# Kernel tuning notes

Hardware: AMD Instinct MI355X
Metric: run time of the kernel (lower is better)

## Reference

```python
import jax, jax.numpy as jnp
import numpy as np


def setup_inputs() -> dict:
    key = jax.random.key(0)
    k_x, k_w, k_b = jax.random.split(key, 3)
    B, Cin, H, W = 32, 256, 56, 56
    Cout, KH, KW = 256, 3, 3
    x = jax.random.normal(k_x, (B, Cin, H, W), dtype=jnp.float32)
    fp_weight = jax.random.normal(k_w, (Cout, Cin, KH, KW), dtype=jnp.float32)
    # binary quantization, conv_mode='input_ch': per-output-channel scale
    scaling_factors = jnp.mean(jnp.abs(fp_weight), axis=(1, 2, 3), keepdims=True)  # [Cout,1,1,1]
    quant_weights = jnp.sign(fp_weight)  # values in {-1,0,1}
    bias = jax.random.normal(k_b, (Cout,), dtype=jnp.float32)
    return {"x": x, "scaling_factors": scaling_factors,
            "quant_weights": quant_weights, "bias": bias}


def reference(x, scaling_factors, quant_weights, bias):
    # Dequantize: per-out-channel scale times sign weights
    new_weights = scaling_factors * quant_weights  # [Cout,Cin,3,3]
    out = jax.lax.conv_general_dilated(
        x, new_weights,
        window_strides=(1, 1),
        padding=((1, 1), (1, 1)),
        dimension_numbers=("NCHW", "OIHW", "NCHW"),
    )
    return out + bias[None, :, None, None]
```

## Files before the change

### kernel.cpp

```cpp
#include <hip/hip_runtime.h>

using half8   = __attribute__((ext_vector_type(8))) _Float16;
using floatx4 = __attribute__((ext_vector_type(4))) float;
using floatx2 = __attribute__((ext_vector_type(2))) float;
using short8  = __attribute__((ext_vector_type(8))) short;

#define XT_ROW_ELEMS 2560
#define XT_ROW_BYTES 5120
#define XT_OFF ((size_t)2 << 20)
#define XT_BYTES ((size_t)256 * 58 * XT_ROW_BYTES)

__device__ __forceinline__ void dma16(const void* g, void* l) {
  __builtin_amdgcn_global_load_lds(
      (const __attribute__((address_space(1))) void*)g,
      (__attribute__((address_space(3))) void*)l, 16, 0, 0);
}

__global__ __launch_bounds__(256) void prep_kernel(
    const float* __restrict__ x, const float* __restrict__ qw,
    _Float16* __restrict__ wre, _Float16* __restrict__ xt)
{
  const int bid = blockIdx.x;
  const int t = threadIdx.x;
  if (bid >= 14848) {
    int idx = (bid - 14848) * 256 + t;
    int c = idx & 255, co = (idx >> 8) & 255, s = idx >> 16;
    wre[idx] = (_Float16)qw[(co * 256 + c) * 9 + s];
    return;
  }
  __shared__ _Float16 lt[32 * 57];
  const int hh = bid % 58;
  const int bc = bid / 58;
  const int cc = bc & 7, b = bc >> 3;
  _Float16* dst = xt + ((size_t)bc * 58 + hh) * XT_ROW_ELEMS;
  const bool interior = (hh >= 1) && (hh <= 56);
  if (interior) {
    const int c = t >> 3, j = t & 7;
    const float* src = x + (((size_t)(b * 256 + cc * 32 + c)) * 56 + (hh - 1)) * 56 + j * 7;
#pragma unroll
    for (int i = 0; i < 7; ++i) lt[c * 57 + j * 7 + i] = (_Float16)src[i];
  }
  __syncthreads();
  for (int ch = t; ch < 320; ch += 256) {
    int pos = ch / 5, sl = ch - pos * 5;
    short8 v = {0, 0, 0, 0, 0, 0, 0, 0};
    if (interior && sl < 4 && pos >= 1 && pos <= 56) {
      int w = pos - 1;
#pragma unroll
      for (int i = 0; i < 8; ++i)
        v[i] = __builtin_bit_cast(short, lt[(sl * 8 + i) * 57 + w]);
    }
    *reinterpret_cast<short8*>(dst + ch * 8) = v;
  }
}

__global__ __launch_bounds__(256, 4) void binconv_v3(
    const float* __restrict__ scale, const float* __restrict__ bias,
    const _Float16* __restrict__ wre, const _Float16* __restrict__ xt,
    float* __restrict__ out)
{
  __shared__ _Float16 xs[2 * 4 * 64 * 40];

  const int tid    = threadIdx.x;
  const int bid    = blockIdx.x;
  const int cohalf = bid & 1;
  const int nb     = bid >> 1;
  const int b      = nb / 28;
  const int h0     = (nb % 28) * 2;
  const int wave   = tid >> 6;
  const int lane   = tid & 63;
  const int nl     = lane & 15;
  const int quad   = lane >> 4;
  const int co_wave = cohalf * 128 + wave * 32;

  int bbase[7];
#pragma unroll
  for (int j = 0; j < 7; ++j) {
    int n = j * 16 + nl;
    int r = (n >= 56) ? 1 : 0;
    int w = n - r * 56;
    bbase[j] = (r * 64 + w) * 80 + quad * 16;
  }

  const _Float16* aptr[2];
#pragma unroll
  for (int mi = 0; mi < 2; ++mi)
    aptr[mi] = wre + (co_wave + mi * 16 + nl) * 256 + quad * 8;

  floatx4 acc[2][7];
#pragma unroll
  for (int mi = 0; mi < 2; ++mi)
#pragma unroll
    for (int j = 0; j < 7; ++j)
      acc[mi][j] = (floatx4){0.f, 0.f, 0.f, 0.f};

  const char* xsrc = (const char*)(xt + ((size_t)(b * 8) * 58 + h0) * XT_ROW_ELEMS);
  const int wlane = wave * XT_ROW_BYTES + lane * 16;
  const int wldso = wave * XT_ROW_BYTES;

#pragma unroll
  for (int i = 0; i < 5; ++i)
    dma16(xsrc + wlane + i * 1024, (char*)xs + wldso + i * 1024);

  int bufoff = 0;
  for (int cc = 0; cc < 8; ++cc) {
    __syncthreads();
    if (cc < 7) {
      const char* srcn = xsrc + (size_t)(cc + 1) * (58 * XT_ROW_BYTES);
#pragma unroll
      for (int i = 0; i < 5; ++i)
        dma16(srcn + wlane + i * 1024,
              (char*)xs + (bufoff ^ 20480) + wldso + i * 1024);
    }
    const int c0 = cc * 32;
    const char* xb = (const char*)xs + bufoff;
    __builtin_amdgcn_s_setprio(1);
#pragma unroll
    for (int s = 0; s < 9; ++s) {
      const int kh = s / 3, kw = s - kh * 3;
      half8 a[2];
#pragma unroll
      for (int mi = 0; mi < 2; ++mi)
        a[mi] = *reinterpret_cast<const half8*>(aptr[mi] + s * 65536 + c0);
      const int soff = (kh * 64 + kw) * 80;
#pragma unroll
      for (int j = 0; j < 7; ++j) {
        half8 bf = *reinterpret_cast<const half8*>(xb + bbase[j] + soff);
#pragma unroll
        for (int mi = 0; mi < 2; ++mi)
          acc[mi][j] = __builtin_amdgcn_mfma_f32_16x16x32_f16(a[mi], bf, acc[mi][j], 0, 0, 0);
      }
    }
    __builtin_amdgcn_s_setprio(0);
    bufoff ^= 20480;
  }

#pragma unroll
  for (int mi = 0; mi < 2; ++mi) {
#pragma unroll
    for (int reg = 0; reg < 4; ++reg) {
      int co = co_wave + mi * 16 + quad * 4 + reg;
      float s_ = scale[co];
      float bi = bias[co];
#pragma unroll
      for (int j = 0; j < 7; ++j) {
        int n = j * 16 + nl;
        int r = (n >= 56) ? 1 : 0;
        int w = n - r * 56;
        out[(((size_t)b * 256 + co) * 56 + (h0 + r)) * 56 + w] =
            acc[mi][j][reg] * s_ + bi;
      }
    }
  }
}

__global__ void repack_weights(const float* __restrict__ qw,
                               _Float16* __restrict__ wre, int n) {
  int t = blockIdx.x * 256 + threadIdx.x;
  if (t >= n) return;
  int c = t & 255, co = (t >> 8) & 255, s = t >> 16;
  wre[t] = (_Float16)qw[(co * 256 + c) * 9 + s];
}

__global__ __launch_bounds__(512, 4) void binconv_fused(
    const float* __restrict__ x, const float* __restrict__ scale,
    const float* __restrict__ bias, const _Float16* __restrict__ wre,
    float* __restrict__ out)
{
  __shared__ _Float16 xs[2 * 4 * 64 * 40];
  const int tid  = threadIdx.x;
  const int nb   = blockIdx.x;
  const int b    = nb / 28;
  const int h0   = (nb % 28) * 2;
  const int wave = tid >> 6;
  const int lane = tid & 63;
  const int nl   = lane & 15;
  const int quad = lane >> 4;
  const int co_wave = wave * 32;
  {
    short8 z = {0, 0, 0, 0, 0, 0, 0, 0};
    short8* xs8 = reinterpret_cast<short8*>(xs);
#pragma unroll
    for (int i = 0; i < 5; ++i) xs8[tid + i * 512] = z;
  }
  const int r     = wave >> 1;
  const int chalf = wave & 1;
  const int sc    = lane & 15;
  const int q     = lane >> 4;
  const int ch    = chalf * 16 + sc;
  const int w0    = q * 14;
  const int h     = h0 + r - 1;
  const bool hok  = (h >= 0) && (h < 56);
  const float* xc = x + (((size_t)b * 256 + ch) * 56 + (hok ? h : 0)) * 56 + w0;
  _Float16* const wrow = xs + r * 2560 + ch;
  floatx2 va[7];
  int bbase[7];
#pragma unroll
  for (int j = 0; j < 7; ++j) {
    int n = j * 16 + nl;
    int rr = (n >= 56) ? 1 : 0;
    int w = n - rr * 56;
    bbase[j] = (rr * 64 + w) * 80 + quad * 16;
  }
  const _Float16* aptr[2];
#pragma unroll
  for (int mi = 0; mi < 2; ++mi)
    aptr[mi] = wre + (co_wave + mi * 16 + nl) * 256 + quad * 8;
  floatx4 acc[2][7];
#pragma unroll
  for (int mi = 0; mi < 2; ++mi)
#pragma unroll
    for (int j = 0; j < 7; ++j)
      acc[mi][j] = (floatx4){0.f, 0.f, 0.f, 0.f};
  __syncthreads();
  if (hok) {
#pragma unroll
    for (int i = 0; i < 7; ++i)
      va[i] = *reinterpret_cast<const floatx2*>(xc + 2 * i);
#pragma unroll
    for (int i = 0; i < 7; ++i) {
      wrow[(w0 + 2 * i + 1) * 40] = (_Float16)va[i][0];
      wrow[(w0 + 2 * i + 2) * 40] = (_Float16)va[i][1];
    }
  }
  int bufe = 0;
  for (int cc = 0; cc < 8; ++cc) {
    __syncthreads();
    if (cc < 7 && hok) {
      const float* A = xc + (size_t)(cc + 1) * 100352;
#pragma unroll
      for (int i = 0; i < 7; ++i)
        va[i] = *reinterpret_cast<const floatx2*>(A + 2 * i);
    }
    const int c0 = cc * 32;
    const char* xb = reinterpret_cast<const char*>(xs) + bufe * 2;
#pragma unroll
    for (int s = 0; s < 9; ++s) {
      const int kh = s / 3, kw = s - kh * 3;
      half8 a[2];
#pragma unroll
      for (int mi = 0; mi < 2; ++mi)
        a[mi] = *reinterpret_cast<const half8*>(aptr[mi] + s * 65536 + c0);
      const int soff = (kh * 64 + kw) * 80;
#pragma unroll
      for (int j = 0; j < 7; ++j) {
        half8 bf = *reinterpret_cast<const half8*>(xb + bbase[j] + soff);
#pragma unroll
        for (int mi = 0; mi < 2; ++mi)
          acc[mi][j] = __builtin_amdgcn_mfma_f32_16x16x32_f16(a[mi], bf, acc[mi][j], 0, 0, 0);
      }
    }
    if (cc < 7 && hok) {
      _Float16* d = wrow + (bufe ^ 10240);
#pragma unroll
      for (int i = 0; i < 7; ++i) {
        d[(w0 + 2 * i + 1) * 40] = (_Float16)va[i][0];
        d[(w0 + 2 * i + 2) * 40] = (_Float16)va[i][1];
      }
    }
    bufe ^= 10240;
  }
#pragma unroll
  for (int mi = 0; mi < 2; ++mi) {
#pragma unroll
    for (int reg = 0; reg < 4; ++reg) {
      int co = co_wave + mi * 16 + quad * 4 + reg;
      float s_ = scale[co];
      float bi = bias[co];
#pragma unroll
      for (int j = 0; j < 7; ++j) {
        int n = j * 16 + nl;
        int rr = (n >= 56) ? 1 : 0;
        int w = n - rr * 56;
        out[(((size_t)b * 256 + co) * 56 + (h0 + rr)) * 56 + w] =
            acc[mi][j][reg] * s_ + bi;
      }
    }
  }
}

extern "C" void kernel_launch(void* const* d_in, const int* in_sizes, int n_in,
                              void* d_out, int out_size, void* d_ws, size_t ws_size,
                              hipStream_t stream) {
  const float* x     = (const float*)d_in[0];
  const float* scale = (const float*)d_in[1];
  const float* qw    = (const float*)d_in[2];
  const float* bias  = (const float*)d_in[3];
  float* out = (float*)d_out;

  _Float16* wre = (_Float16*)d_ws;

  if (ws_size >= XT_OFF + XT_BYTES) {
    _Float16* xt = (_Float16*)((char*)d_ws + XT_OFF);
    prep_kernel<<<17152, 256, 0, stream>>>(x, qw, wre, xt);
    binconv_v3<<<1792, 256, 0, stream>>>(scale, bias, wre, xt, out);
  } else {
    repack_weights<<<2304, 256, 0, stream>>>(qw, wre, 9 * 256 * 256);
    binconv_fused<<<896, 512, 0, stream>>>(x, scale, bias, wre, out);
  }
}
```

Baseline: 341.2 us.

## Double per-wave output-channel tile and software-pipeline operand loads in binconv

Each block now covers all 256 output channels (64 per wave) instead of splitting them across two blocks, so every LDS input tile is staged once and reused across twice as many MFMAs. The grid is halved and launch bounds drop to 2 blocks per SM to make room for the larger accumulator set. The weight and LDS operand loads are also prefetched one kernel tap ahead into register double-buffers, overlapping them with the MFMAs of the current tap. The cost is higher register pressure and lower occupancy, and the 896-block grid may fill the 256 CUs unevenly.

```diff
diff --git a/kernel.cpp b/kernel.cpp
--- a/kernel.cpp
+++ b/kernel.cpp
@@ -54,24 +54,22 @@
   }
 }
 
-__global__ __launch_bounds__(256, 4) void binconv_v3(
+__global__ __launch_bounds__(256, 2) void binconv_v4(
     const float* __restrict__ scale, const float* __restrict__ bias,
     const _Float16* __restrict__ wre, const _Float16* __restrict__ xt,
     float* __restrict__ out)
 {
   __shared__ _Float16 xs[2 * 4 * 64 * 40];
 
-  const int tid    = threadIdx.x;
-  const int bid    = blockIdx.x;
-  const int cohalf = bid & 1;
-  const int nb     = bid >> 1;
-  const int b      = nb / 28;
-  const int h0     = (nb % 28) * 2;
-  const int wave   = tid >> 6;
-  const int lane   = tid & 63;
-  const int nl     = lane & 15;
-  const int quad   = lane >> 4;
-  const int co_wave = cohalf * 128 + wave * 32;
+  const int tid  = threadIdx.x;
+  const int nb   = blockIdx.x;
+  const int b    = nb / 28;
+  const int h0   = (nb % 28) * 2;
+  const int wave = tid >> 6;
+  const int lane = tid & 63;
+  const int nl   = lane & 15;
+  const int quad = lane >> 4;
+  const int co_wave = wave * 64;
 
   int bbase[7];
 #pragma unroll
@@ -82,14 +80,14 @@
     bbase[j] = (r * 64 + w) * 80 + quad * 16;
   }
 
-  const _Float16* aptr[2];
-#pragma unroll
-  for (int mi = 0; mi < 2; ++mi)
+  const _Float16* aptr[4];
+#pragma unroll
+  for (int mi = 0; mi < 4; ++mi)
     aptr[mi] = wre + (co_wave + mi * 16 + nl) * 256 + quad * 8;
 
-  floatx4 acc[2][7];
-#pragma unroll
-  for (int mi = 0; mi < 2; ++mi)
+  floatx4 acc[4][7];
+#pragma unroll
+  for (int mi = 0; mi < 4; ++mi)
 #pragma unroll
     for (int j = 0; j < 7; ++j)
       acc[mi][j] = (floatx4){0.f, 0.f, 0.f, 0.f};
@@ -101,6 +99,11 @@
 #pragma unroll
   for (int i = 0; i < 5; ++i)
     dma16(xsrc + wlane + i * 1024, (char*)xs + wldso + i * 1024);
+
+  half8 acur[4], anxt[4];
+#pragma unroll
+  for (int mi = 0; mi < 4; ++mi)
+    acur[mi] = *reinterpret_cast<const half8*>(aptr[mi]);
 
   int bufoff = 0;
   for (int cc = 0; cc < 8; ++cc) {
@@ -114,29 +117,45 @@
     }
     const int c0 = cc * 32;
     const char* xb = (const char*)xs + bufoff;
-    __builtin_amdgcn_s_setprio(1);
+
+    half8 bcur[7], bnxt[7];
+#pragma unroll
+    for (int j = 0; j < 7; ++j)
+      bcur[j] = *reinterpret_cast<const half8*>(xb + bbase[j]);
+
 #pragma unroll
     for (int s = 0; s < 9; ++s) {
-      const int kh = s / 3, kw = s - kh * 3;
-      half8 a[2];
-#pragma unroll
-      for (int mi = 0; mi < 2; ++mi)
-        a[mi] = *reinterpret_cast<const half8*>(aptr[mi] + s * 65536 + c0);
-      const int soff = (kh * 64 + kw) * 80;
-#pragma unroll
-      for (int j = 0; j < 7; ++j) {
-        half8 bf = *reinterpret_cast<const half8*>(xb + bbase[j] + soff);
-#pragma unroll
-        for (int mi = 0; mi < 2; ++mi)
-          acc[mi][j] = __builtin_amdgcn_mfma_f32_16x16x32_f16(a[mi], bf, acc[mi][j], 0, 0, 0);
-      }
-    }
-    __builtin_amdgcn_s_setprio(0);
+      if (s < 8) {
+        const int kh1 = (s + 1) / 3, kw1 = (s + 1) - kh1 * 3;
+        const int soff1 = (kh1 * 64 + kw1) * 80;
+#pragma unroll
+        for (int j = 0; j < 7; ++j)
+          bnxt[j] = *reinterpret_cast<const half8*>(xb + bbase[j] + soff1);
+      }
+      if (cc < 7 || s < 8) {
+        const int s1 = (s < 8) ? s + 1 : 0;
+        const int c1 = (s < 8) ? c0 : c0 + 32;
+#pragma unroll
+        for (int mi = 0; mi < 4; ++mi)
+          anxt[mi] = *reinterpret_cast<const half8*>(aptr[mi] + s1 * 65536 + c1);
+      }
+      __builtin_amdgcn_s_setprio(1);
+#pragma unroll
+      for (int j = 0; j < 7; ++j)
+#pragma unroll
+        for (int mi = 0; mi < 4; ++mi)
+          acc[mi][j] = __builtin_amdgcn_mfma_f32_16x16x32_f16(acur[mi], bcur[j], acc[mi][j], 0, 0, 0);
+      __builtin_amdgcn_s_setprio(0);
+#pragma unroll
+      for (int mi = 0; mi < 4; ++mi) acur[mi] = anxt[mi];
+#pragma unroll
+      for (int j = 0; j < 7; ++j) bcur[j] = bnxt[j];
+    }
     bufoff ^= 20480;
   }
 
 #pragma unroll
-  for (int mi = 0; mi < 2; ++mi) {
+  for (int mi = 0; mi < 4; ++mi) {
 #pragma unroll
     for (int reg = 0; reg < 4; ++reg) {
       int co = co_wave + mi * 16 + quad * 4 + reg;
@@ -293,7 +312,7 @@
   if (ws_size >= XT_OFF + XT_BYTES) {
     _Float16* xt = (_Float16*)((char*)d_ws + XT_OFF);
     prep_kernel<<<17152, 256, 0, stream>>>(x, qw, wre, xt);
-    binconv_v3<<<1792, 256, 0, stream>>>(scale, bias, wre, xt, out);
+    binconv_v4<<<896, 256, 0, stream>>>(scale, bias, wre, xt, out);
   } else {
     repack_weights<<<2304, 256, 0, stream>>>(qw, wre, 9 * 256 * 256);
     binconv_fused<<<896, 512, 0, stream>>>(x, scale, bias, wre, out);
```

Result: faster. 329.6 us (-3.4%).
